# Performance work log

Hardware: AMD Instinct MI355X
Metric: run time of the kernel (lower is better)

Reference implementation:

```python
import jax, jax.numpy as jnp
import numpy as np

B, V, G, D = 16, 16384, 20000, 64


def setup_inputs() -> dict:
    key = jax.random.key(0)
    k1, k2 = jax.random.split(key)
    variant_embeddings = jax.random.normal(k1, (B, V, D), dtype=jnp.float32)
    gene_ids = jax.random.randint(k2, (B, V), 0, G, dtype=jnp.int64)
    mask = jnp.ones((B, V), dtype=bool)
    return {
        "variant_embeddings": variant_embeddings,
        "gene_ids": gene_ids,
        "mask": mask,
        "num_genes": G,
    }


def reference(variant_embeddings, gene_ids, mask, num_genes):
    # Aggregation = 'max'. Genes with no valid variants -> zero embedding.
    b, v, d = variant_embeddings.shape
    # Flatten (batch, variant) and build per-(batch,gene) segment ids.
    seg = (jnp.arange(b, dtype=gene_ids.dtype)[:, None] * num_genes + gene_ids).reshape(-1)
    m = mask.reshape(-1)
    # Route padded variants to a dummy trailing segment so they never contribute.
    dummy = b * num_genes
    seg = jnp.where(m, seg, dummy)
    x = variant_embeddings.reshape(b * v, d)  # mask-zeroing is a no-op for selected (valid) rows under max
    num_segments = b * num_genes + 1
    mx = jax.ops.segment_max(x, seg, num_segments=num_segments)[: b * num_genes]  # [b*G, d]
    counts = jax.ops.segment_sum(m.astype(x.dtype), seg, num_segments=num_segments)[: b * num_genes]  # [b*G]
    out = jnp.where(counts[:, None] > 0, mx, jnp.zeros((), dtype=x.dtype))
    return out.reshape(b, num_genes, d)
```

## Files before the change

kernel.cpp:

```cpp
#include <hip/hip_runtime.h>

constexpr int B = 16;
constexpr int V = 16384;
constexpr int G = 20000;
constexpr int D = 64;
constexpr int NCELLS = B * G;
constexpr int NROWS  = B * V;
constexpr int OVF_MAX = 16384;
constexpr long long OUT_N = (long long)NCELLS * D;

typedef float f32x4 __attribute__((ext_vector_type(4)));

constexpr int HDR_WORDS = 4 * NCELLS;
constexpr int OVF_HDR   = HDR_WORDS;
constexpr int OVF_LIST  = HDR_WORDS + 1;
constexpr int SPILL_OFF = HDR_WORDS + 1 + 2 * OVF_MAX;

__global__ void ga_zero(uint4* __restrict__ ws4, unsigned int* __restrict__ ws) {
  int stride = gridDim.x * blockDim.x;
  for (int i = blockIdx.x * blockDim.x + threadIdx.x; i < HDR_WORDS / 4; i += stride)
    ws4[i] = make_uint4(0u, 0u, 0u, 0u);
  if (blockIdx.x == 0 && threadIdx.x == 0) ws[OVF_HDR] = 0u;
}

__global__ void ga_build(const int* __restrict__ gene_ids,
                         const int* __restrict__ mask,
                         unsigned int* __restrict__ ws, int scap) {
  int r = blockIdx.x * blockDim.x + threadIdx.x;
  if (r >= NROWS) return;
  if (!mask[r]) return;
  int cell = (r >> 14) * G + gene_ids[r];
  unsigned int pos = atomicAdd(&ws[cell * 4], 1u);
  if (pos < 3u) {
    ws[cell * 4 + 1 + pos] = (unsigned int)r;
  } else if (pos < 3u + (unsigned int)scap) {
    ws[SPILL_OFF + (size_t)cell * scap + (pos - 3u)] = (unsigned int)r;
  } else {
    unsigned int o = atomicAdd(&ws[OVF_HDR], 1u);
    if (o < (unsigned int)OVF_MAX) {
      ws[OVF_LIST + 2 * o + 0] = (unsigned int)cell;
      ws[OVF_LIST + 2 * o + 1] = (unsigned int)r;
    }
  }
}

__device__ __forceinline__ void fmax4(f32x4& a, f32x4 v) {
  a.x = fmaxf(a.x, v.x);
  a.y = fmaxf(a.y, v.y);
  a.z = fmaxf(a.z, v.z);
  a.w = fmaxf(a.w, v.w);
}

constexpr int CPT = 8;
__global__ void ga_gather(const f32x4* __restrict__ emb4,
                          const uint4* __restrict__ hdr,
                          const unsigned int* __restrict__ spill,
                          f32x4* __restrict__ out4, int scap) {
  const int STRIDE = NCELLS / CPT;
  int t = blockIdx.x * blockDim.x + threadIdx.x;
  int cell0 = t >> 4;
  int sub   = t & 15;
  if (cell0 >= STRIDE) return;

  uint4 h[CPT];
#pragma unroll
  for (int k = 0; k < CPT; ++k)
    h[k] = hdr[cell0 + k * STRIDE];

  f32x4 v0[CPT], v1[CPT], v2[CPT];
#pragma unroll
  for (int k = 0; k < CPT; ++k) {
    unsigned int c  = h[k].x;
    unsigned int r0 = c ? h[k].y : 0u;
    unsigned int r1 = (c >= 2u) ? h[k].z : r0;
    unsigned int r2 = (c >= 3u) ? h[k].w : r0;
    v0[k] = emb4[(size_t)r0 * 16 + sub];
    v1[k] = emb4[(size_t)r1 * 16 + sub];
    v2[k] = emb4[(size_t)r2 * 16 + sub];
  }

#pragma unroll
  for (int k = 0; k < CPT; ++k) {
    int cell = cell0 + k * STRIDE;
    unsigned int c = h[k].x;
    f32x4 acc = v0[k];
    fmax4(acc, v1[k]);
    fmax4(acc, v2[k]);
    if (c > 3u) {
      int n1 = (int)c - 3; if (n1 > scap) n1 = scap;
      const unsigned int* sp = spill + (size_t)cell * scap;
      for (int j = 0; j < n1; ++j)
        fmax4(acc, emb4[(size_t)sp[j] * 16 + sub]);
    }
    acc.x = c ? acc.x : 0.f;
    acc.y = c ? acc.y : 0.f;
    acc.z = c ? acc.z : 0.f;
    acc.w = c ? acc.w : 0.f;
    __builtin_nontemporal_store(acc, &out4[(size_t)cell * 16 + sub]);
  }
}

__device__ __forceinline__ void atomic_max_float(float* addr, float val) {
  unsigned int* ua = (unsigned int*)addr;
  unsigned int old = *ua;
  while (__uint_as_float(old) < val) {
    unsigned int assumed = old;
    old = atomicCAS(ua, assumed, __float_as_uint(val));
    if (old == assumed) break;
  }
}

__global__ void ga_ovf(const f32x4* __restrict__ emb4,
                       const unsigned int* __restrict__ ws,
                       float* __restrict__ out) {
  unsigned int nov = ws[OVF_HDR];
  if (nov > (unsigned int)OVF_MAX) nov = OVF_MAX;
  int total = (int)nov * 16;
  int stride = gridDim.x * blockDim.x;
  for (int u = blockIdx.x * blockDim.x + threadIdx.x; u < total; u += stride) {
    int e = u >> 4, sub = u & 15;
    unsigned int cell = ws[OVF_LIST + 2 * e + 0];
    unsigned int row  = ws[OVF_LIST + 2 * e + 1];
    f32x4 v = emb4[(size_t)row * 16 + sub];
    float* o = out + (size_t)cell * 64 + sub * 4;
    atomic_max_float(o + 0, v.x);
    atomic_max_float(o + 1, v.y);
    atomic_max_float(o + 2, v.z);
    atomic_max_float(o + 3, v.w);
  }
}

__device__ __forceinline__ unsigned int enc_f32(float f) {
  unsigned int u = __float_as_uint(f);
  return (u & 0x80000000u) ? ~u : (u | 0x80000000u);
}
__device__ __forceinline__ float dec_f32(unsigned int e) {
  unsigned int u = (e & 0x80000000u) ? (e ^ 0x80000000u) : ~e;
  return __uint_as_float(u);
}

__global__ void ga_init(uint4* __restrict__ out4, int n4) {
  int stride = gridDim.x * blockDim.x;
  for (int i = blockIdx.x * blockDim.x + threadIdx.x; i < n4; i += stride)
    out4[i] = make_uint4(0u, 0u, 0u, 0u);
}

__global__ void ga_scatter(const float4* __restrict__ emb4,
                           const int* __restrict__ gene_ids,
                           const int* __restrict__ mask,
                           unsigned int* __restrict__ out) {
  int tid = blockIdx.x * blockDim.x + threadIdx.x;
  int v  = tid >> 4;
  int dq = tid & 15;
  if (!mask[v]) return;
  int g = gene_ids[v];
  int b = v >> 14;
  float4 e = emb4[tid];
  int base = (b * G + g) * D + (dq << 2);
  atomicMax(out + base + 0, enc_f32(e.x));
  atomicMax(out + base + 1, enc_f32(e.y));
  atomicMax(out + base + 2, enc_f32(e.z));
  atomicMax(out + base + 3, enc_f32(e.w));
}

__global__ void ga_finalize(uint4* __restrict__ io4, int n4) {
  int stride = gridDim.x * blockDim.x;
  for (int i = blockIdx.x * blockDim.x + threadIdx.x; i < n4; i += stride) {
    uint4 e = io4[i];
    float4 f;
    f.x = e.x ? dec_f32(e.x) : 0.0f;
    f.y = e.y ? dec_f32(e.y) : 0.0f;
    f.z = e.z ? dec_f32(e.z) : 0.0f;
    f.w = e.w ? dec_f32(e.w) : 0.0f;
    *reinterpret_cast<float4*>(io4 + i) = f;
  }
}

extern "C" void kernel_launch(void* const* d_in, const int* in_sizes, int n_in,
                              void* d_out, int out_size, void* d_ws, size_t ws_size,
                              hipStream_t stream) {
  const float4* emb4     = (const float4*)d_in[0];
  const int*    gene_ids = (const int*)d_in[1];
  const int*    mask     = (const int*)d_in[2];

  long long ws_u32 = (long long)(ws_size / 4);
  long long avail  = ws_u32 - (long long)SPILL_OFF;
  int scap = (int)(avail > 0 ? avail / NCELLS : -1);
  if (scap > 13) scap = 13;

  if (scap >= 0) {
    unsigned int* ws = (unsigned int*)d_ws;
    ga_zero<<<1024, 256, 0, stream>>>((uint4*)d_ws, ws);
    ga_build<<<NROWS / 256, 256, 0, stream>>>(gene_ids, mask, ws, scap);
    const int N = (NCELLS / CPT) * 16;
    ga_gather<<<N / 256, 256, 0, stream>>>(
        (const f32x4*)emb4, (const uint4*)d_ws, ws + SPILL_OFF,
        (f32x4*)d_out, scap);
    ga_ovf<<<64, 256, 0, stream>>>((const f32x4*)emb4, ws, (float*)d_out);
  } else {
    unsigned int* out_u = (unsigned int*)d_out;
    const int n4 = (int)(OUT_N / 4);
    ga_init<<<2048, 256, 0, stream>>>((uint4*)d_out, n4);
    ga_scatter<<<(NROWS * 16) / 256, 256, 0, stream>>>(emb4, gene_ids, mask, out_u);
    ga_finalize<<<2048, 256, 0, stream>>>((uint4*)d_out, n4);
  }
}
```

Measured before the change: 49.34 us.

## Map gather blocks to batches per XCD for L2 locality of embedding rows

```diff
diff --git a/kernel.cpp b/kernel.cpp
--- a/kernel.cpp
+++ b/kernel.cpp
@@ -52,26 +52,38 @@
 }
 
 constexpr int CPT = 8;
+constexpr int CELLS_PER_BLOCK  = (256 / 16) * CPT;
+constexpr int BLOCKS_PER_BATCH = (G + CELLS_PER_BLOCK - 1) / CELLS_PER_BLOCK;
+constexpr int GATHER_BLOCKS    = BLOCKS_PER_BATCH * B;
+
 __global__ void ga_gather(const f32x4* __restrict__ emb4,
                           const uint4* __restrict__ hdr,
                           const unsigned int* __restrict__ spill,
                           f32x4* __restrict__ out4, int scap) {
-  const int STRIDE = NCELLS / CPT;
-  int t = blockIdx.x * blockDim.x + threadIdx.x;
-  int cell0 = t >> 4;
-  int sub   = t & 15;
-  if (cell0 >= STRIDE) return;
+  int j   = blockIdx.x;
+  int xcd = j & 7;
+  int jj  = j >> 3;
+  int half  = (jj >= BLOCKS_PER_BATCH) ? 1 : 0;
+  int local = jj - half * BLOCKS_PER_BATCH;
+  int batch = xcd + 8 * half;
+
+  int gi  = threadIdx.x >> 4;
+  int sub = threadIdx.x & 15;
+  int cidx0 = local * CELLS_PER_BLOCK + gi;
 
   uint4 h[CPT];
 #pragma unroll
-  for (int k = 0; k < CPT; ++k)
-    h[k] = hdr[cell0 + k * STRIDE];
+  for (int k = 0; k < CPT; ++k) {
+    int cidx = cidx0 + k * 16;
+    int cc   = cidx < G ? cidx : G - 1;
+    h[k] = hdr[(size_t)batch * G + cc];
+  }
 
   f32x4 v0[CPT], v1[CPT], v2[CPT];
 #pragma unroll
   for (int k = 0; k < CPT; ++k) {
     unsigned int c  = h[k].x;
-    unsigned int r0 = c ? h[k].y : 0u;
+    unsigned int r0 = c ? h[k].y : (unsigned int)(batch * V);
     unsigned int r1 = (c >= 2u) ? h[k].z : r0;
     unsigned int r2 = (c >= 3u) ? h[k].w : r0;
     v0[k] = emb4[(size_t)r0 * 16 + sub];
@@ -81,22 +93,24 @@
 
 #pragma unroll
   for (int k = 0; k < CPT; ++k) {
-    int cell = cell0 + k * STRIDE;
+    int cidx = cidx0 + k * 16;
+    if (cidx >= G) continue;
+    size_t cell = (size_t)batch * G + cidx;
     unsigned int c = h[k].x;
     f32x4 acc = v0[k];
     fmax4(acc, v1[k]);
     fmax4(acc, v2[k]);
     if (c > 3u) {
       int n1 = (int)c - 3; if (n1 > scap) n1 = scap;
-      const unsigned int* sp = spill + (size_t)cell * scap;
-      for (int j = 0; j < n1; ++j)
-        fmax4(acc, emb4[(size_t)sp[j] * 16 + sub]);
+      const unsigned int* sp = spill + cell * scap;
+      for (int jx = 0; jx < n1; ++jx)
+        fmax4(acc, emb4[(size_t)sp[jx] * 16 + sub]);
     }
     acc.x = c ? acc.x : 0.f;
     acc.y = c ? acc.y : 0.f;
     acc.z = c ? acc.z : 0.f;
     acc.w = c ? acc.w : 0.f;
-    __builtin_nontemporal_store(acc, &out4[(size_t)cell * 16 + sub]);
+    __builtin_nontemporal_store(acc, &out4[cell * 16 + sub]);
   }
 }
 
@@ -192,8 +206,7 @@
     unsigned int* ws = (unsigned int*)d_ws;
     ga_zero<<<1024, 256, 0, stream>>>((uint4*)d_ws, ws);
     ga_build<<<NROWS / 256, 256, 0, stream>>>(gene_ids, mask, ws, scap);
-    const int N = (NCELLS / CPT) * 16;
-    ga_gather<<<N / 256, 256, 0, stream>>>(
+    ga_gather<<<GATHER_BLOCKS, 256, 0, stream>>>(
         (const f32x4*)emb4, (const uint4*)d_ws, ws + SPILL_OFF,
         (f32x4*)d_out, scap);
     ga_ovf<<<64, 256, 0, stream>>>((const f32x4*)emb4, ws, (float*)d_out);
```

Result: slower. 53.60 us (+8.6%).
